# Performance work log

Measured on AMD Instinct MI355X. Metric: run time of the kernel, lower is better.

## Reference

```python
import jax, jax.numpy as jnp
import numpy as np

NUM_GROUPS = 32
EPS = 1e-4
N_HEADS = 8


def group_norm(x, w, b):
    # x: [B, C, L]; normalize over (channels-in-group, L)
    bsz, c, l = x.shape
    xg = x.reshape(bsz, NUM_GROUPS, c // NUM_GROUPS, l)
    mu = jnp.mean(xg, axis=(2, 3), keepdims=True)
    var = jnp.var(xg, axis=(2, 3), keepdims=True)
    xn = ((xg - mu) * jax.lax.rsqrt(var + EPS)).reshape(bsz, c, l)
    return xn * w[None, :, None] + b[None, :, None]


def setup_inputs() -> dict:
    key = jax.random.key(0)
    ks = jax.random.split(key, 7)
    B, C, H, W = 16, 512, 32, 32
    return {
        "x": jax.random.normal(ks[0], (B, C, H, W), dtype=jnp.float32),
        "norm_w": jax.random.uniform(ks[1], (C,), dtype=jnp.float32, minval=0.5, maxval=1.5),
        "norm_b": jax.random.normal(ks[2], (C,), dtype=jnp.float32) * 0.1,
        "qkv_w": jax.random.normal(ks[3], (3 * C, C), dtype=jnp.float32) * (1.0 / np.sqrt(C)),
        "qkv_b": jax.random.normal(ks[4], (3 * C,), dtype=jnp.float32) * 0.02,
        "proj_w": jax.random.normal(ks[5], (C, C), dtype=jnp.float32) * (1.0 / np.sqrt(C)),
        "proj_b": jax.random.normal(ks[6], (C,), dtype=jnp.float32) * 0.02,
    }


def reference(x, norm_w, norm_b, qkv_w, qkv_b, proj_w, proj_b):
    b, c, hh, ww = x.shape
    l = hh * ww
    xf = x.reshape(b, c, l)
    # GroupNorm + 1x1 conv (pointwise) -> qkv: [B, 3C, L]
    qkv = jnp.einsum('oc,bcl->bol', qkv_w, group_norm(xf, norm_w, norm_b)) + qkv_b[None, :, None]
    ch = c // N_HEADS
    q, k, v = jnp.split(qkv, 3, axis=1)
    q = q.reshape(b * N_HEADS, ch, l)
    k = k.reshape(b * N_HEADS, ch, l)
    v = v.reshape(b * N_HEADS, ch, l)
    scale = ch ** -0.25
    # full O(L^2) attention matrix, as in OldQKVAttention
    weight = jnp.einsum('bct,bcs->bts', q * scale, k * scale)
    weight = jax.nn.softmax(weight, axis=-1)
    a = jnp.einsum('bts,bcs->bct', weight, v).reshape(b, c, l)
    h = jnp.einsum('oc,bcl->bol', proj_w, a) + proj_b[None, :, None]
    return (xf + h).reshape(b, c, hh, ww)
```

## Files before the change

kernel.cpp:

```cpp
#include <hip/hip_runtime.h>
#include <cmath>


#define BATCH 16
#define CDIM 512
#define LDIM 1024
#define NQ (786432u)
#define NP (262144u)

#define AS1 __attribute__((address_space(1)))
#define AS3 __attribute__((address_space(3)))

typedef unsigned short u16;
typedef u16 ushort8v __attribute__((ext_vector_type(8)));
typedef __bf16 bf16x8_t __attribute__((ext_vector_type(8)));
typedef float f32x4 __attribute__((ext_vector_type(4)));

__device__ __forceinline__ u16 f2bf(float f) {
  unsigned u = __float_as_uint(f);
  unsigned r = u + 0x7fffu + ((u >> 16) & 1u);
  return (u16)(r >> 16);
}
__device__ __forceinline__ unsigned pack2(float a, float b) {
  return (unsigned)f2bf(a) | ((unsigned)f2bf(b) << 16);
}
__device__ __forceinline__ unsigned pack2t(float a, float b) {
  return __builtin_amdgcn_perm(__float_as_uint(b), __float_as_uint(a), 0x07060302u);
}
__device__ __forceinline__ float bftrunc(float x) {
  return __uint_as_float(__float_as_uint(x) & 0xffff0000u);
}
__device__ __forceinline__ float fast_exp2(float x) {
#if __has_builtin(__builtin_amdgcn_exp2f)
  return __builtin_amdgcn_exp2f(x);
#else
  return exp2f(x);
#endif
}
__device__ __forceinline__ f32x4 mfma16(ushort8v a, ushort8v b, f32x4 c) {
  return __builtin_amdgcn_mfma_f32_16x16x32_bf16(
      __builtin_bit_cast(bf16x8_t, a), __builtin_bit_cast(bf16x8_t, b), c, 0, 0, 0);
}
__device__ __forceinline__ void g2l16(const u16* g, u16* l) {
  __builtin_amdgcn_global_load_lds((const AS1 void*)g, (AS3 void*)l, 16, 0, 0);
}

__global__ __launch_bounds__(256) void gn_stats_kernel(const float* __restrict__ x,
                                                       const float* __restrict__ w,
                                                       const float* __restrict__ bvec,
                                                       float* __restrict__ scl,
                                                       float* __restrict__ sh) {
  int bg = blockIdx.x;
  int bb = bg >> 5, g = bg & 31;
  size_t base = ((size_t)bb * CDIM + g * 16) * LDIM;
  const float4* x4 = (const float4*)(x + base);
  int tid = threadIdx.x;
  float sum = 0.f, ss = 0.f;
#pragma unroll
  for (int i = 0; i < 16; ++i) {
    float4 v = x4[tid + 256 * i];
    sum += v.x + v.y + v.z + v.w;
    ss += v.x * v.x + v.y * v.y + v.z * v.z + v.w * v.w;
  }
#pragma unroll
  for (int off = 32; off; off >>= 1) {
    sum += __shfl_xor(sum, off);
    ss += __shfl_xor(ss, off);
  }
  __shared__ float rs[4], rq[4];
  int lane = tid & 63, wv = tid >> 6;
  if (lane == 0) { rs[wv] = sum; rq[wv] = ss; }
  __syncthreads();
  sum = rs[0] + rs[1] + rs[2] + rs[3];
  ss = rq[0] + rq[1] + rq[2] + rq[3];
  const float inv_n = 1.f / (16.f * 1024.f);
  float mean = sum * inv_n;
  float var = ss * inv_n - mean * mean;
  float rstd = rsqrtf(var + 1e-4f);
  if (tid < 16) {
    int c = g * 16 + tid;
    float s = w[c] * rstd;
    scl[bb * CDIM + c] = s;
    sh[bb * CDIM + c] = bvec[c] - mean * s;
  }
}

__global__ __launch_bounds__(256) void wpack_kernel(const float* __restrict__ wq,
                                                    const float* __restrict__ wp,
                                                    u16* __restrict__ wqb,
                                                    u16* __restrict__ wpb) {
  size_t i = (size_t)blockIdx.x * 2048 + (size_t)threadIdx.x * 8;
  const float* sp;
  u16* dp;
  size_t off;
  if (i < NQ) {
    off = i;
    sp = wq;
    dp = wqb;
  } else {
    off = i - NQ;
    sp = wp;
    dp = wpb;
  }
  float4 a = *(const float4*)&sp[off];
  float4 b = *(const float4*)&sp[off + 4];
  uint4 o;
  o.x = pack2(a.x, a.y);
  o.y = pack2(a.z, a.w);
  o.z = pack2(b.x, b.y);
  o.w = pack2(b.z, b.w);
  *(uint4*)&dp[off] = o;
}

__global__ __launch_bounds__(256) void xpose_kernel(const float* __restrict__ x,
                                                    const float* __restrict__ scl,
                                                    const float* __restrict__ sh,
                                                    u16* __restrict__ xnT) {
  __shared__ u16 T[64][72];
  int b = blockIdx.z, c0 = blockIdx.y * 64, l0 = blockIdx.x * 64;
  int tid = threadIdx.x;
  int ci = tid >> 4, ljs = (tid & 15) * 4;
#pragma unroll
  for (int rep = 0; rep < 4; ++rep) {
    int c = rep * 16 + ci;
    float s_ = scl[b * CDIM + c0 + c];
    float h_ = sh[b * CDIM + c0 + c];
    float4 v = *(const float4*)&x[((size_t)b * CDIM + c0 + c) * LDIM + l0 + ljs];
    T[ljs + 0][c] = f2bf(v.x * s_ + h_);
    T[ljs + 1][c] = f2bf(v.y * s_ + h_);
    T[ljs + 2][c] = f2bf(v.z * s_ + h_);
    T[ljs + 3][c] = f2bf(v.w * s_ + h_);
  }
  __syncthreads();
  int lr = tid >> 2, cs8 = (tid & 3) * 16;
  uint4 o0 = *(const uint4*)&T[lr][cs8];
  uint4 o1 = *(const uint4*)&T[lr][cs8 + 8];
  size_t dst = ((size_t)b * LDIM + l0 + lr) * CDIM + c0 + cs8;
  *(uint4*)&xnT[dst] = o0;
  *(uint4*)&xnT[dst + 8] = o1;
}

template <int MODE>
__global__ __launch_bounds__(256) void gemm_mfma(
    const u16* __restrict__ Wb, const float* __restrict__ biasg,
    const u16* __restrict__ Xt, const float* __restrict__ resid,
    u16* __restrict__ qo, u16* __restrict__ ko,
    u16* __restrict__ vo, float* __restrict__ fo) {
  __shared__ __align__(16) u16 As_[128][32];
  __shared__ __align__(16) u16 Xs_[128][32];
  int bb = blockIdx.z;
  int m0 = blockIdx.y * 128;
  int n0 = blockIdx.x * 128;
  int tid = threadIdx.x;
  int w = tid >> 6, lane = tid & 63, quad = lane >> 4, l15 = lane & 15;
  int wm = (w >> 1) * 64, wn = (w & 1) * 64;
  int srow = lane >> 2, scol = (lane & 3) * 8;
  const u16* Xb = Xt + (size_t)bb * LDIM * CDIM;
  f32x4 acc[4][4] = {};
  bool qkpath = (MODE == 0) && (m0 < 1024);

  for (int kk = 0; kk < 512; kk += 32) {
#pragma unroll
    for (int r = 0; r < 2; ++r) {
      int row = w * 32 + r * 16;
      g2l16(&Wb[(size_t)(m0 + row + srow) * 512 + kk + scol], &As_[row][0]);
      g2l16(&Xb[(size_t)(n0 + row + srow) * 512 + kk + scol], &Xs_[row][0]);
    }
    __syncthreads();
    ushort8v af[4], bfr[4];
#pragma unroll
    for (int i = 0; i < 4; ++i) af[i] = *(const ushort8v*)&As_[wm + i * 16 + l15][quad * 8];
#pragma unroll
    for (int i = 0; i < 4; ++i) bfr[i] = *(const ushort8v*)&Xs_[wn + i * 16 + l15][quad * 8];
    if (qkpath) {
#pragma unroll
      for (int i = 0; i < 4; ++i)
#pragma unroll
        for (int j = 0; j < 4; ++j) acc[j][i] = mfma16(bfr[j], af[i], acc[j][i]);
    } else {
#pragma unroll
      for (int i = 0; i < 4; ++i)
#pragma unroll
        for (int j = 0; j < 4; ++j) acc[i][j] = mfma16(af[i], bfr[j], acc[i][j]);
    }
    __syncthreads();
  }

  if (MODE == 0 && m0 < 1024) {
    bool isQ = (m0 < 512);
    float qscale = isQ ? (0.125f * 1.44269504f) : 1.0f;
    u16* dst = isQ ? qo : ko;
    int cbase0 = m0 - (isQ ? 0 : 512) + wm;
#pragma unroll
    for (int i = 0; i < 4; ++i) {
      int cg = cbase0 + i * 16 + l15;
      float bv = biasg[m0 + wm + i * 16 + l15];
      int hh = cg >> 6, cl = cg & 63;
      size_t rowbase = ((size_t)(bb * 8 + hh) * 1024) * 64 + cl;
#pragma unroll
      for (int j = 0; j < 4; ++j)
#pragma unroll
        for (int r = 0; r < 4; ++r) {
          int t = n0 + wn + j * 16 + quad * 4 + r;
          dst[rowbase + (size_t)t * 64] = f2bf((acc[j][i][r] + bv) * qscale);
        }
    }
  } else if (MODE == 0) {
#pragma unroll
    for (int i = 0; i < 4; ++i)
#pragma unroll
      for (int r = 0; r < 4; ++r) {
        int m_abs = m0 + wm + i * 16 + quad * 4 + r;
        float bv = biasg[m_abs];
        int cg = m_abs - 1024;
#pragma unroll
        for (int j = 0; j < 4; ++j) {
          int n = n0 + wn + j * 16 + l15;
          vo[((size_t)bb * CDIM + cg) * LDIM + n] = f2bf(acc[i][j][r] + bv);
        }
      }
  } else {
#pragma unroll
    for (int i = 0; i < 4; ++i)
#pragma unroll
      for (int r = 0; r < 4; ++r) {
        int m_abs = m0 + wm + i * 16 + quad * 4 + r;
        float bv = biasg[m_abs];
#pragma unroll
        for (int j = 0; j < 4; ++j) {
          int n = n0 + wn + j * 16 + l15;
          size_t off = ((size_t)bb * CDIM + m_abs) * LDIM + n;
          fo[off] = acc[i][j][r] + bv + resid[off];
        }
      }
  }
}

__global__ __launch_bounds__(256) void attn_mfma(const u16* __restrict__ qt,
                                                 const u16* __restrict__ kt,
                                                 const u16* __restrict__ vv,
                                                 u16* __restrict__ avT) {
  __shared__ __align__(16) u16 Ks[2][32][72];
  __shared__ __align__(16) u16 Vs[2][64][40];
  __shared__ __align__(16) u16 Ps[4][32][40];
  __shared__ float linv[4][32];
  int bh = blockIdx.x;
  int t0b = blockIdx.y * 128;
  int b = bh >> 3, h = bh & 7;
  int tid = threadIdx.x;
  int w = tid >> 6, lane = tid & 63, quad = lane >> 4, l15 = lane & 15;
  int t0w = t0b + w * 32;
  size_t head = (size_t)bh * 65536;
  const u16* kbase = kt + head;
  const u16* vbase = vv + head;

  int sK = tid >> 3, cK8 = (tid & 7) * 8;
  int cV = tid >> 2, sV8 = (tid & 3) * 8;

  ushort8v qf[2][2];
#pragma unroll
  for (int ts = 0; ts < 2; ++ts)
#pragma unroll
    for (int kc = 0; kc < 2; ++kc)
      qf[ts][kc] =
          *(const ushort8v*)&qt[head + (size_t)(t0w + ts * 16 + l15) * 64 + kc * 32 + quad * 8];

  f32x4 Co[2][4] = {};
  float lacc[2] = {0.f, 0.f};

  {
    uint4 k0 = *(const uint4*)&kbase[(size_t)tid * 8];
    uint4 v0 = *(const uint4*)&vbase[(size_t)cV * 1024 + sV8];
    *(uint4*)&Ks[0][sK][cK8] = k0;
    *(uint4*)&Vs[0][cV][sV8] = v0;
  }
  __syncthreads();

  int cur = 0;
  for (int ci = 0; ci < 32; ++ci) {
    int sn = ((ci + 1) & 31) * 32;
    uint4 kn = *(const uint4*)&kbase[(size_t)sn * 64 + tid * 8];
    uint4 vn = *(const uint4*)&vbase[(size_t)cV * 1024 + sn + sV8];

    ushort8v kf[2][2];
#pragma unroll
    for (int ms = 0; ms < 2; ++ms)
#pragma unroll
      for (int kc = 0; kc < 2; ++kc)
        kf[ms][kc] = *(const ushort8v*)&Ks[cur][ms * 16 + l15][kc * 32 + quad * 8];
    ushort8v vf[4];
#pragma unroll
    for (int cs = 0; cs < 4; ++cs) vf[cs] = *(const ushort8v*)&Vs[cur][cs * 16 + l15][quad * 8];

    f32x4 st[2][2];
#pragma unroll
    for (int ts = 0; ts < 2; ++ts)
#pragma unroll
      for (int ms = 0; ms < 2; ++ms) {
        f32x4 z = {};
        z = mfma16(kf[ms][0], qf[ts][0], z);
        st[ts][ms] = mfma16(kf[ms][1], qf[ts][1], z);
      }
#pragma unroll
    for (int ts = 0; ts < 2; ++ts) {
      float p0 = fast_exp2(st[ts][0].x), p1 = fast_exp2(st[ts][0].y);
      float p2 = fast_exp2(st[ts][0].z), p3 = fast_exp2(st[ts][0].w);
      float p4 = fast_exp2(st[ts][1].x), p5 = fast_exp2(st[ts][1].y);
      float p6 = fast_exp2(st[ts][1].z), p7 = fast_exp2(st[ts][1].w);
      lacc[ts] += ((bftrunc(p0) + bftrunc(p1)) + (bftrunc(p2) + bftrunc(p3))) +
                  ((bftrunc(p4) + bftrunc(p5)) + (bftrunc(p6) + bftrunc(p7)));
      uint2 u0, u1;
      u0.x = pack2t(p0, p1);
      u0.y = pack2t(p2, p3);
      u1.x = pack2t(p4, p5);
      u1.y = pack2t(p6, p7);
      *(uint2*)&Ps[w][ts * 16 + l15][quad * 4] = u0;
      *(uint2*)&Ps[w][ts * 16 + l15][16 + quad * 4] = u1;
    }
    ushort8v pb[2];
#pragma unroll
    for (int ts = 0; ts < 2; ++ts) pb[ts] = *(const ushort8v*)&Ps[w][ts * 16 + l15][quad * 8];
#pragma unroll
    for (int ts = 0; ts < 2; ++ts)
#pragma unroll
      for (int cs = 0; cs < 4; ++cs) Co[ts][cs] = mfma16(pb[ts], vf[cs], Co[ts][cs]);

    int nxt = cur ^ 1;
    *(uint4*)&Ks[nxt][sK][cK8] = kn;
    *(uint4*)&Vs[nxt][cV][sV8] = vn;
    __syncthreads();
    cur = nxt;
  }

#pragma unroll
  for (int ts = 0; ts < 2; ++ts) {
    lacc[ts] += __shfl_xor(lacc[ts], 16);
    lacc[ts] += __shfl_xor(lacc[ts], 32);
    if (quad == 0) linv[w][ts * 16 + l15] = 1.f / lacc[ts];
  }
#pragma unroll
  for (int ts = 0; ts < 2; ++ts)
#pragma unroll
    for (int r = 0; r < 4; ++r) {
      int tl = ts * 16 + quad * 4 + r;
      float iv = linv[w][tl];
      size_t rowb = ((size_t)b * LDIM + t0w + tl) * CDIM + h * 64;
#pragma unroll
      for (int cs = 0; cs < 4; ++cs)
        avT[rowb + cs * 16 + l15] = f2bf(Co[ts][cs][r] * iv);
    }
}

extern "C" void kernel_launch(void* const* d_in, const int* in_sizes, int n_in,
                              void* d_out, int out_size, void* d_ws, size_t ws_size,
                              hipStream_t stream) {
  const float* x = (const float*)d_in[0];
  const float* norm_w = (const float*)d_in[1];
  const float* norm_b = (const float*)d_in[2];
  const float* qkv_w = (const float*)d_in[3];
  const float* qkv_b = (const float*)d_in[4];
  const float* proj_w = (const float*)d_in[5];
  const float* proj_b = (const float*)d_in[6];
  float* out = (float*)d_out;

  const size_t NE = (size_t)BATCH * CDIM * LDIM;
  float* scl = (float*)d_ws;
  float* sh = scl + BATCH * CDIM;
  u16* qt = (u16*)(sh + BATCH * CDIM);
  u16* kt = qt + NE;
  u16* vv = kt + NE;
  u16* av = vv + NE;
  u16* xn = av + NE;
  u16* wqb = xn + NE;
  u16* wpb = wqb + NQ;

  gn_stats_kernel<<<dim3(BATCH * 32), dim3(256), 0, stream>>>(x, norm_w, norm_b, scl, sh);
  wpack_kernel<<<dim3((NQ + NP) / 2048), dim3(256), 0, stream>>>(qkv_w, proj_w, wqb, wpb);
  xpose_kernel<<<dim3(16, 8, BATCH), dim3(256), 0, stream>>>(x, scl, sh, xn);
  gemm_mfma<0><<<dim3(8, 12, BATCH), dim3(256), 0, stream>>>(
      wqb, qkv_b, xn, (const float*)nullptr, qt, kt, vv, (float*)nullptr);
  attn_mfma<<<dim3(128, 8), dim3(256), 0, stream>>>(qt, kt, vv, av);
  gemm_mfma<1><<<dim3(8, 4, BATCH), dim3(256), 0, stream>>>(
      wpb, proj_b, av, x, (u16*)nullptr, (u16*)nullptr, (u16*)nullptr, out);
}
```

Baseline: 213.9 us.

## Use direct global-to-LDS loads with XOR swizzle and MFMA row sums in attention

The attention kernel now stages K and V tiles through global_load_lds straight into unpadded, XOR-swizzled LDS buffers instead of loading into registers and storing. The softmax denominator is accumulated with an extra MFMA against a ones vector, which replaces the scalar bf16-truncated sums and the shuffle reduction. GroupNorm statistics and weight packing are also merged into one prep kernel to save a launch. The swizzle has to line up exactly with how the direct-to-LDS load places each lane's 16 bytes, so a mismatch would give wrong results, and the extra MFMA adds matrix-core work.

```diff
diff --git a/kernel.cpp b/kernel.cpp
--- a/kernel.cpp
+++ b/kernel.cpp
@@ -26,9 +26,6 @@
 }
 __device__ __forceinline__ unsigned pack2t(float a, float b) {
   return __builtin_amdgcn_perm(__float_as_uint(b), __float_as_uint(a), 0x07060302u);
-}
-__device__ __forceinline__ float bftrunc(float x) {
-  return __uint_as_float(__float_as_uint(x) & 0xffff0000u);
 }
 __device__ __forceinline__ float fast_exp2(float x) {
 #if __has_builtin(__builtin_amdgcn_exp2f)
@@ -45,71 +42,72 @@
   __builtin_amdgcn_global_load_lds((const AS1 void*)g, (AS3 void*)l, 16, 0, 0);
 }
 
-__global__ __launch_bounds__(256) void gn_stats_kernel(const float* __restrict__ x,
-                                                       const float* __restrict__ w,
-                                                       const float* __restrict__ bvec,
-                                                       float* __restrict__ scl,
-                                                       float* __restrict__ sh) {
-  int bg = blockIdx.x;
-  int bb = bg >> 5, g = bg & 31;
-  size_t base = ((size_t)bb * CDIM + g * 16) * LDIM;
-  const float4* x4 = (const float4*)(x + base);
+__global__ __launch_bounds__(256) void prep_kernel(const float* __restrict__ x,
+                                                   const float* __restrict__ w,
+                                                   const float* __restrict__ bvec,
+                                                   const float* __restrict__ wq,
+                                                   const float* __restrict__ wp,
+                                                   float* __restrict__ scl,
+                                                   float* __restrict__ sh,
+                                                   u16* __restrict__ wqb,
+                                                   u16* __restrict__ wpb) {
   int tid = threadIdx.x;
-  float sum = 0.f, ss = 0.f;
-#pragma unroll
-  for (int i = 0; i < 16; ++i) {
-    float4 v = x4[tid + 256 * i];
-    sum += v.x + v.y + v.z + v.w;
-    ss += v.x * v.x + v.y * v.y + v.z * v.z + v.w * v.w;
-  }
-#pragma unroll
-  for (int off = 32; off; off >>= 1) {
-    sum += __shfl_xor(sum, off);
-    ss += __shfl_xor(ss, off);
-  }
-  __shared__ float rs[4], rq[4];
-  int lane = tid & 63, wv = tid >> 6;
-  if (lane == 0) { rs[wv] = sum; rq[wv] = ss; }
-  __syncthreads();
-  sum = rs[0] + rs[1] + rs[2] + rs[3];
-  ss = rq[0] + rq[1] + rq[2] + rq[3];
-  const float inv_n = 1.f / (16.f * 1024.f);
-  float mean = sum * inv_n;
-  float var = ss * inv_n - mean * mean;
-  float rstd = rsqrtf(var + 1e-4f);
-  if (tid < 16) {
-    int c = g * 16 + tid;
-    float s = w[c] * rstd;
-    scl[bb * CDIM + c] = s;
-    sh[bb * CDIM + c] = bvec[c] - mean * s;
-  }
-}
-
-__global__ __launch_bounds__(256) void wpack_kernel(const float* __restrict__ wq,
-                                                    const float* __restrict__ wp,
-                                                    u16* __restrict__ wqb,
-                                                    u16* __restrict__ wpb) {
-  size_t i = (size_t)blockIdx.x * 2048 + (size_t)threadIdx.x * 8;
-  const float* sp;
-  u16* dp;
-  size_t off;
-  if (i < NQ) {
-    off = i;
-    sp = wq;
-    dp = wqb;
+  if (blockIdx.x < 512) {
+    int bg = blockIdx.x;
+    int bb = bg >> 5, g = bg & 31;
+    size_t base = ((size_t)bb * CDIM + g * 16) * LDIM;
+    const float4* x4 = (const float4*)(x + base);
+    float sum = 0.f, ss = 0.f;
+#pragma unroll
+    for (int i = 0; i < 16; ++i) {
+      float4 v = x4[tid + 256 * i];
+      sum += v.x + v.y + v.z + v.w;
+      ss += v.x * v.x + v.y * v.y + v.z * v.z + v.w * v.w;
+    }
+#pragma unroll
+    for (int off = 32; off; off >>= 1) {
+      sum += __shfl_xor(sum, off);
+      ss += __shfl_xor(ss, off);
+    }
+    __shared__ float rs[4], rq[4];
+    int lane = tid & 63, wv = tid >> 6;
+    if (lane == 0) { rs[wv] = sum; rq[wv] = ss; }
+    __syncthreads();
+    sum = rs[0] + rs[1] + rs[2] + rs[3];
+    ss = rq[0] + rq[1] + rq[2] + rq[3];
+    const float inv_n = 1.f / (16.f * 1024.f);
+    float mean = sum * inv_n;
+    float var = ss * inv_n - mean * mean;
+    float rstd = rsqrtf(var + 1e-4f);
+    if (tid < 16) {
+      int c = g * 16 + tid;
+      float s = w[c] * rstd;
+      scl[bb * CDIM + c] = s;
+      sh[bb * CDIM + c] = bvec[c] - mean * s;
+    }
   } else {
-    off = i - NQ;
-    sp = wp;
-    dp = wpb;
-  }
-  float4 a = *(const float4*)&sp[off];
-  float4 b = *(const float4*)&sp[off + 4];
-  uint4 o;
-  o.x = pack2(a.x, a.y);
-  o.y = pack2(a.z, a.w);
-  o.z = pack2(b.x, b.y);
-  o.w = pack2(b.z, b.w);
-  *(uint4*)&dp[off] = o;
+    size_t i = (size_t)(blockIdx.x - 512) * 2048 + (size_t)tid * 8;
+    const float* sp;
+    u16* dp;
+    size_t off;
+    if (i < NQ) {
+      off = i;
+      sp = wq;
+      dp = wqb;
+    } else {
+      off = i - NQ;
+      sp = wp;
+      dp = wpb;
+    }
+    float4 a = *(const float4*)&sp[off];
+    float4 b = *(const float4*)&sp[off + 4];
+    uint4 o;
+    o.x = pack2(a.x, a.y);
+    o.y = pack2(a.z, a.w);
+    o.z = pack2(b.x, b.y);
+    o.w = pack2(b.z, b.w);
+    *(uint4*)&dp[off] = o;
+  }
 }
 
 __global__ __launch_bounds__(256) void xpose_kernel(const float* __restrict__ x,
@@ -240,8 +238,8 @@
                                                  const u16* __restrict__ kt,
                                                  const u16* __restrict__ vv,
                                                  u16* __restrict__ avT) {
-  __shared__ __align__(16) u16 Ks[2][32][72];
-  __shared__ __align__(16) u16 Vs[2][64][40];
+  __shared__ __align__(16) u16 Ks[2][32][64];
+  __shared__ __align__(16) u16 Vs[2][64][32];
   __shared__ __align__(16) u16 Ps[4][32][40];
   __shared__ float linv[4][32];
   int bh = blockIdx.x;
@@ -254,8 +252,12 @@
   const u16* kbase = kt + head;
   const u16* vbase = vv + head;
 
-  int sK = tid >> 3, cK8 = (tid & 7) * 8;
-  int cV = tid >> 2, sV8 = (tid & 3) * 8;
+  int sK = tid >> 3;
+  int gKseg = (tid & 7) ^ (sK & 7);
+  int cV = tid >> 2;
+  int gVseg = (tid & 3) ^ ((tid >> 3) & 3);
+  u16* ldsK[2] = {&Ks[0][(w * 8)][0], &Ks[1][(w * 8)][0]};
+  u16* ldsV[2] = {&Vs[0][(w * 16)][0], &Vs[1][(w * 16)][0]};
 
   ushort8v qf[2][2];
 #pragma unroll
@@ -265,32 +267,39 @@
       qf[ts][kc] =
           *(const ushort8v*)&qt[head + (size_t)(t0w + ts * 16 + l15) * 64 + kc * 32 + quad * 8];
 
+  ushort8v ones;
+#pragma unroll
+  for (int i = 0; i < 8; ++i) ones[i] = 0x3F80;
+
   f32x4 Co[2][4] = {};
-  float lacc[2] = {0.f, 0.f};
-
-  {
-    uint4 k0 = *(const uint4*)&kbase[(size_t)tid * 8];
-    uint4 v0 = *(const uint4*)&vbase[(size_t)cV * 1024 + sV8];
-    *(uint4*)&Ks[0][sK][cK8] = k0;
-    *(uint4*)&Vs[0][cV][sV8] = v0;
-  }
+  f32x4 Ls[2] = {};
+
+  g2l16(&kbase[(size_t)sK * 64 + gKseg * 8], ldsK[0]);
+  g2l16(&vbase[(size_t)cV * 1024 + gVseg * 8], ldsV[0]);
   __syncthreads();
 
   int cur = 0;
   for (int ci = 0; ci < 32; ++ci) {
     int sn = ((ci + 1) & 31) * 32;
-    uint4 kn = *(const uint4*)&kbase[(size_t)sn * 64 + tid * 8];
-    uint4 vn = *(const uint4*)&vbase[(size_t)cV * 1024 + sn + sV8];
+    int nxt = cur ^ 1;
+    g2l16(&kbase[(size_t)(sn + sK) * 64 + gKseg * 8], ldsK[nxt]);
+    g2l16(&vbase[(size_t)cV * 1024 + sn + gVseg * 8], ldsV[nxt]);
 
     ushort8v kf[2][2];
 #pragma unroll
     for (int ms = 0; ms < 2; ++ms)
 #pragma unroll
-      for (int kc = 0; kc < 2; ++kc)
-        kf[ms][kc] = *(const ushort8v*)&Ks[cur][ms * 16 + l15][kc * 32 + quad * 8];
+      for (int kc = 0; kc < 2; ++kc) {
+        int s = ms * 16 + l15;
+        int seg = kc * 4 + quad;
+        kf[ms][kc] = *(const ushort8v*)&Ks[cur][s][(seg ^ (s & 7)) * 8];
+      }
     ushort8v vf[4];
 #pragma unroll
-    for (int cs = 0; cs < 4; ++cs) vf[cs] = *(const ushort8v*)&Vs[cur][cs * 16 + l15][quad * 8];
+    for (int cs = 0; cs < 4; ++cs) {
+      int c = cs * 16 + l15;
+      vf[cs] = *(const ushort8v*)&Vs[cur][c][(quad ^ ((c >> 1) & 3)) * 8];
+    }
 
     f32x4 st[2][2];
 #pragma unroll
@@ -307,8 +316,6 @@
       float p2 = fast_exp2(st[ts][0].z), p3 = fast_exp2(st[ts][0].w);
       float p4 = fast_exp2(st[ts][1].x), p5 = fast_exp2(st[ts][1].y);
       float p6 = fast_exp2(st[ts][1].z), p7 = fast_exp2(st[ts][1].w);
-      lacc[ts] += ((bftrunc(p0) + bftrunc(p1)) + (bftrunc(p2) + bftrunc(p3))) +
-                  ((bftrunc(p4) + bftrunc(p5)) + (bftrunc(p6) + bftrunc(p7)));
       uint2 u0, u1;
       u0.x = pack2t(p0, p1);
       u0.y = pack2t(p2, p3);
@@ -321,23 +328,19 @@
 #pragma unroll
     for (int ts = 0; ts < 2; ++ts) pb[ts] = *(const ushort8v*)&Ps[w][ts * 16 + l15][quad * 8];
 #pragma unroll
-    for (int ts = 0; ts < 2; ++ts)
+    for (int ts = 0; ts < 2; ++ts) {
 #pragma unroll
       for (int cs = 0; cs < 4; ++cs) Co[ts][cs] = mfma16(pb[ts], vf[cs], Co[ts][cs]);
-
-    int nxt = cur ^ 1;
-    *(uint4*)&Ks[nxt][sK][cK8] = kn;
-    *(uint4*)&Vs[nxt][cV][sV8] = vn;
+      Ls[ts] = mfma16(ones, pb[ts], Ls[ts]);
+    }
+
     __syncthreads();
     cur = nxt;
   }
 
 #pragma unroll
-  for (int ts = 0; ts < 2; ++ts) {
-    lacc[ts] += __shfl_xor(lacc[ts], 16);
-    lacc[ts] += __shfl_xor(lacc[ts], 32);
-    if (quad == 0) linv[w][ts * 16 + l15] = 1.f / lacc[ts];
-  }
+  for (int ts = 0; ts < 2; ++ts)
+    if (quad == 0) linv[w][ts * 16 + l15] = 1.f / Ls[ts][0];
 #pragma unroll
   for (int ts = 0; ts < 2; ++ts)
 #pragma unroll
@@ -346,8 +349,7 @@
       float iv = linv[w][tl];
       size_t rowb = ((size_t)b * LDIM + t0w + tl) * CDIM + h * 64;
 #pragma unroll
-      for (int cs = 0; cs < 4; ++cs)
-        avT[rowb + cs * 16 + l15] = f2bf(Co[ts][cs][r] * iv);
+      for (int cs = 0; cs < 4; ++cs) avT[rowb + cs * 16 + l15] = f2bf(Co[ts][cs][r] * iv);
     }
 }
 
@@ -374,8 +376,8 @@
   u16* wqb = xn + NE;
   u16* wpb = wqb + NQ;
 
-  gn_stats_kernel<<<dim3(BATCH * 32), dim3(256), 0, stream>>>(x, norm_w, norm_b, scl, sh);
-  wpack_kernel<<<dim3((NQ + NP) / 2048), dim3(256), 0, stream>>>(qkv_w, proj_w, wqb, wpb);
+  prep_kernel<<<dim3(1024), dim3(256), 0, stream>>>(x, norm_w, norm_b, qkv_w, proj_w,
+                                                    scl, sh, wqb, wpb);
   xpose_kernel<<<dim3(16, 8, BATCH), dim3(256), 0, stream>>>(x, scl, sh, xn);
   gemm_mfma<0><<<dim3(8, 12, BATCH), dim3(256), 0, stream>>>(
       wqb, qkv_b, xn, (const float*)nullptr, qt, kt, vv, (float*)nullptr);
```

After: 218.4 us. 2.1% more time.
